# Optimization experiments

Measured on AMD Instinct MI355X. Metric: run time of the kernel, lower is better.

## Reference

```python
import jax, jax.numpy as jnp
import numpy as np

# Grid dimensions (match init_kwargs)
N_G = 100      # generators (grid['n_unit'])
N_LINE = 500   # transmission lines
N_LOAD = 200   # loads
N_BUS = 300    # buses
N_W = 50       # uncertainty sources (num_uncertainties)
N_SCEN = 128   # batch of realized-error scenarios (CvxpyLayer batch dim)
C_VIOL = 2.0e4 # violation penalty c_viol
N_ITERS = 600  # PDHG iterations for the batched LP solve
POWER_ITERS = 50


def _one_hot_nodes(key, n_items, n_bus):
    # incidence matrix [n_bus, n_items]: each item attached to one random bus
    idx = jax.random.randint(key, (n_items,), 0, n_bus)
    return jax.nn.one_hot(idx, n_bus, dtype=jnp.float32).T


def setup_inputs() -> dict:
    key = jax.random.key(0)
    ks = jax.random.split(key, 12)
    Pmax = 1.0 + 4.0 * jax.random.uniform(ks[0], (N_G,), dtype=jnp.float32)
    p_da = 0.8 * Pmax * jax.random.uniform(ks[1], (N_G,), dtype=jnp.float32)
    r_up_hat = jax.random.uniform(ks[2], (N_G,), dtype=jnp.float32)
    r_down_hat = jax.random.uniform(ks[3], (N_G,), dtype=jnp.float32)
    f_margin_up_hat = 5.0 + 5.0 * jax.random.uniform(ks[4], (N_LINE,), dtype=jnp.float32)
    f_margin_down_hat = 5.0 + 5.0 * jax.random.uniform(ks[5], (N_LINE,), dtype=jnp.float32)
    PTDF = 0.2 * jax.random.normal(ks[6], (N_LINE, N_BUS), dtype=jnp.float32)
    node_G = _one_hot_nodes(ks[7], N_G, N_BUS)
    node_L = _one_hot_nodes(ks[8], N_LOAD, N_BUS)
    node_W = _one_hot_nodes(ks[9], N_W, N_BUS)
    w_error_scen = 0.1 * jax.random.normal(ks[10], (N_SCEN, N_W), dtype=jnp.float32)
    return dict(p_da=p_da, r_up_hat=r_up_hat, r_down_hat=r_down_hat,
                f_margin_up_hat=f_margin_up_hat, f_margin_down_hat=f_margin_down_hat,
                w_error_scen=w_error_scen, Pmax=Pmax, PTDF=PTDF,
                node_G=node_G, node_L=node_L, node_W=node_W)


def _rt_clearing(p_da, r_up_hat, r_down_hat, f_up_hat, f_down_hat, w, Pmax, PTDF, node_G, node_L, node_W):
    # --- projection clamps (exactly as in torch forward) ---
    zero = jnp.zeros((), jnp.float32)
    r_up = jnp.maximum(jnp.minimum(r_up_hat, Pmax - p_da), zero)
    r_down = jnp.maximum(jnp.minimum(r_down_hat, p_da), zero)
    f_up = jnp.maximum(f_up_hat, zero)
    f_down = jnp.maximum(f_down_hat, zero)

    # --- reduced flow-sensitivity matrices ---
    Hg = PTDF @ node_G   # [L, G]
    Hl = PTDF @ node_L   # [L, D]
    Hw = PTDF @ node_W   # [L, W]

    G, D, L = N_G, N_LOAD, N_LINE
    n = 3 * G + D                 # x = [r_up_rec, r_down_rec, g_shed, l_shed]
    m = 2 * G + 2 * L + 1         # ineq rows + 1 equality (power balance)

    I = jnp.eye(G, dtype=jnp.float32)
    Zgg = jnp.zeros((G, G), jnp.float32)
    Zgd = jnp.zeros((G, D), jnp.float32)
    row1 = jnp.concatenate([I, Zgg, Zgg, Zgd], axis=1)          # ru <= r_up
    row2 = jnp.concatenate([Zgg, I, Zgg, Zgd], axis=1)          # rd <= r_down
    row3 = jnp.concatenate([Hg, -Hg, -Hg, Hl], axis=1)          # flow up
    row4 = -row3                                                # flow down
    og = jnp.ones((1, G), jnp.float32); od = jnp.ones((1, D), jnp.float32)
    row5 = jnp.concatenate([og, -og, -og, od], axis=1)          # balance (equality)
    K = jnp.concatenate([row1, row2, row3, row4, row5], axis=0)  # [m, n]

    c = C_VIOL * jnp.concatenate([jnp.zeros(2 * G, jnp.float32), jnp.ones(G + D, jnp.float32)])

    # per-scenario RHS q: Kx <= q (rows :-1), Kx == q (last row)
    S = w.shape[0]
    wH = w @ Hw.T  # [S, L]
    q = jnp.concatenate([
        jnp.broadcast_to(r_up, (S, G)),
        jnp.broadcast_to(r_down, (S, G)),
        f_up[None, :] - wH,
        f_down[None, :] + wH,
        -jnp.sum(w, axis=1, keepdims=True),
    ], axis=1)  # [S, m]

    # spectral norm of K via power iteration (step sizes)
    v = jnp.ones((n,), jnp.float32) / np.sqrt(n)
    s = jnp.ones((), jnp.float32)
    for _ in range(POWER_ITERS):
        v = K.T @ (K @ v)
        s = jnp.linalg.norm(v)
        v = v / s
    Lnorm = jnp.sqrt(s)
    step = 0.9 / Lnorm  # tau = sigma = step, tau*sigma*||K||^2 < 1

    ineq_mask = (jnp.arange(m) < m - 1)  # last row is equality: dual unprojected

    def pdhg_step(carry, _):
        x, y = carry
        x1 = jnp.maximum(x - step * (c + y @ K), 0.0)           # primal: x >= 0
        xb = 2.0 * x1 - x
        y1 = y + step * (xb @ K.T - q)
        y1 = jnp.where(ineq_mask, jnp.maximum(y1, 0.0), y1)     # dual: y_ineq >= 0
        return (x1, y1), None

    x0 = jnp.zeros((S, n), jnp.float32)
    y0 = jnp.zeros((S, m), jnp.float32)
    (xf, _), _ = jax.lax.scan(pdhg_step, (x0, y0), None, length=N_ITERS)

    g_shed = xf[:, 2 * G:3 * G]
    l_shed = xf[:, 3 * G:]
    cost_RT = C_VIOL * (jnp.sum(g_shed, axis=1) + jnp.sum(l_shed, axis=1))
    return cost_RT[:, None]  # [S, 1], matches cvxpy cost_RT variable


def reference(p_da, r_up_hat, r_down_hat, f_margin_up_hat, f_margin_down_hat,
              w_error_scen, Pmax, PTDF, node_G, node_L, node_W):
    return _rt_clearing(p_da, r_up_hat, r_down_hat, f_margin_up_hat, f_margin_down_hat,
                        w_error_scen, Pmax, PTDF, node_G, node_L, node_W)
```

## Files before the change

### kernel.cpp

```cpp
#include <hip/hip_runtime.h>
#include <hip/hip_fp16.h>
#include <math.h>

#define NG 100
#define ND 200
#define NLINE 500
#define NB 300
#define NW 50
#define NS 128
#define NX 500
#define CVIOL 20000.0f
#define NITERS 600
#define PITERS 50
#define NUPAD_MAX 304

#define NC   13
#define NUC  208

#define OFF_HSPB 0
#define OFF_HST  114688
#define OFF_B    270336
#define OFF_HWT  360336
#define OFF_QC   385336
#define OFF_QD   449336
#define OFF_RUP  513336
#define OFF_RDN  513436
#define OFF_FUP  513536
#define OFF_FDN  514036
#define OFF_QE   514536
#define OFF_STEP 514664
#define OFF_NU   514665
#define OFF_NUP  514666
#define OFF_NUC  514667
#define OFF_BUS  514668
#define OFF_BUSW 514968
#define OFF_UBUS 515018
#define OFF_C2U  515322
#define OFF_CUS  515622
#define OFF_CUL  515927

union f16pair { unsigned int u; _Float16 h[2]; };
__device__ __forceinline__ float h2lo(unsigned int x){ f16pair p; p.u = x; return (float)p.h[0]; }
__device__ __forceinline__ float h2hi(unsigned int x){ f16pair p; p.u = x; return (float)p.h[1]; }

__global__ __launch_bounds__(512) void k_pre(
    const float* __restrict__ p_da, const float* __restrict__ r_up_hat,
    const float* __restrict__ r_down_hat, const float* __restrict__ fup_hat,
    const float* __restrict__ fdn_hat, const float* __restrict__ w_err,
    const float* __restrict__ Pmax, const float* __restrict__ nG,
    const float* __restrict__ nL, const float* __restrict__ nW, float* ws) {
  __shared__ int busL[NB];
  __shared__ int uidxL[NB];
  __shared__ int cntL[NUPAD_MAX];
  __shared__ int ubusL[NUPAD_MAX];
  __shared__ int c2uL[NB];
  __shared__ int cusL[NUPAD_MAX + 1];
  __shared__ int culL[NB];
  const int t = threadIdx.x;
  int* busW = (int*)(ws + OFF_BUSW);
  if (t < NG) {
    int bf = 0;
    for (int b = 0; b < NB; ++b) if (nG[b*NG + t] > 0.5f) bf = b;
    busL[t] = bf;
    ws[OFF_RUP + t] = fmaxf(fminf(r_up_hat[t], Pmax[t] - p_da[t]), 0.f);
    ws[OFF_RDN + t] = fmaxf(fminf(r_down_hat[t], p_da[t]), 0.f);
  }
  if (t < ND) {
    int bf = 0;
    for (int b = 0; b < NB; ++b) if (nL[b*ND + t] > 0.5f) bf = b;
    busL[NG + t] = bf;
  }
  if (t < NW) {
    int bf = 0;
    for (int b = 0; b < NB; ++b) if (nW[b*NW + t] > 0.5f) bf = b;
    busW[t] = bf;
  }
  if (t < NLINE) {
    ws[OFF_FUP + t] = fmaxf(fup_hat[t], 0.f);
    ws[OFF_FDN + t] = fmaxf(fdn_hat[t], 0.f);
  }
  if (t < NS) {
    float s = 0.f;
    for (int w = 0; w < NW; ++w) s += w_err[t*NW + w];
    ws[OFF_QE + t] = -s;
  }
  __syncthreads();
  if (t == 0) {
    for (int b = 0; b < NB; ++b) uidxL[b] = -1;
    int nu = 0;
    for (int c = 0; c < NB; ++c) {
      const int b = busL[c];
      if (uidxL[b] < 0) { uidxL[b] = nu; ubusL[nu] = b; nu++; }
      c2uL[c] = uidxL[b];
    }
    for (int u = nu; u < NUPAD_MAX; ++u) ubusL[u] = 0;
    ((int*)(ws + OFF_NU))[0]  = nu;
    ((int*)(ws + OFF_NUP))[0] = (nu + 31) & ~31;
    ((int*)(ws + OFF_NUC))[0] = (nu <= NUC) ? NUC : 0;
    for (int u = 0; u < NUPAD_MAX; ++u) cntL[u] = 0;
    for (int c = 0; c < NB; ++c) cntL[c2uL[c]]++;
    int acc = 0;
    for (int u = 0; u < nu; ++u) { cusL[u] = acc; acc += cntL[u]; cntL[u] = cusL[u]; }
    for (int u = nu; u <= NUPAD_MAX; ++u) { if (u < NUPAD_MAX + 1) cusL[u] = acc; }
    for (int c = 0; c < NB; ++c) culL[cntL[c2uL[c]]++] = c;
  }
  __syncthreads();
  if (t < NUPAD_MAX) ((int*)(ws + OFF_UBUS))[t] = ubusL[t];
  if (t < NUPAD_MAX + 1) ((int*)(ws + OFF_CUS))[t] = cusL[t];
  if (t < NB) {
    ((int*)(ws + OFF_C2U))[t] = c2uL[t];
    ((int*)(ws + OFF_CUL))[t] = culL[t];
  }
}

__global__ __launch_bounds__(512) void k_buildH(const float* __restrict__ PTDF, float* ws) {
  const int l = blockIdx.x;
  const int t = threadIdx.x;
  const int NU   = ((const int*)(ws + OFF_NU))[0];
  const int NUCr = ((const int*)(ws + OFF_NUC))[0];
  const int* ubus = (const int*)(ws + OFF_UBUS);
  const int* busW = (const int*)(ws + OFF_BUSW);
  unsigned short* hb = (unsigned short*)(ws + OFF_HSPB);
  if (t < NUPAD_MAX) {
    const float val = (t < NU) ? PTDF[l*NB + ubus[t]] : 0.f;
    ws[OFF_HST + t*512 + l] = val;
    if (l == 0) {
      for (int ll = NLINE; ll < 512; ++ll) ws[OFF_HST + t*512 + ll] = 0.f;
    }
    if (NUCr > 0 && t < NUCr) {
      const int jp = l >> 6, half = (l >> 5) & 1, rg = l & 31;
      const unsigned short bv = __half_as_ushort(__float2half(val));
      hb[((((jp*NUC + t) << 5) + rg) << 1) + half] = bv;
      if (l == 0) {
        for (int rr = 20; rr < 32; ++rr)
          hb[((((7*NUC + t) << 5) + rr) << 1) + 1] = 0;
      }
    }
  } else if (t < NUPAD_MAX + NW) {
    const int w = t - NUPAD_MAX;
    ws[OFF_HWT + w*NLINE + l] = PTDF[l*NB + busW[w]];
  }
}

__global__ __launch_bounds__(192) void k_buildB(float* ws) {
  const int e = blockIdx.x;
  const int j = threadIdx.x;
  if (j >= 152) return;
  const float* __restrict__ re  = ws + OFF_HST + e*512;
  const float* __restrict__ rf0 = ws + OFF_HST + (2*j)*512;
  const float* __restrict__ rf1 = rf0 + 512;
  float a0 = 0.f, a1 = 0.f;
  #pragma unroll 4
  for (int l = 0; l < NLINE; ++l) {
    const float rv = re[l];
    a0 = fmaf(rv, rf0[l], a0);
    a1 = fmaf(rv, rf1[l], a1);
  }
  const unsigned int pk = (unsigned int)__half_as_ushort(__float2half(a0)) |
                          ((unsigned int)__half_as_ushort(__float2half(a1)) << 16);
  ((unsigned int*)(ws + OFF_B))[e*152 + j] = pk;
}

__global__ __launch_bounds__(512) void k_power(float* ws) {
  __shared__ unsigned int BuL[208*105];
  __shared__ __align__(16) float v[512];
  __shared__ float q3[NB];
  __shared__ __align__(16) float busq[NUPAD_MAX];
  __shared__ float gq[416];
  __shared__ int c2uL[NB], cusL[NUPAD_MAX + 1], culL[NB];
  __shared__ float sEs, sSs;
  const int t = threadIdx.x;
  const int NUCr = ((const int*)(ws + OFF_NUC))[0];
  const bool small = (NUCr == NUC);
  const unsigned int* __restrict__ BuPk = (const unsigned int*)(ws + OFF_B);
  if (small) {
    for (int i = t; i < 208*104; i += 512)
      BuL[(i/104)*105 + (i%104)] = BuPk[(i/104)*152 + (i%104)];
  }
  if (t < NB) { c2uL[t] = ((const int*)(ws + OFF_C2U))[t]; culL[t] = ((const int*)(ws + OFF_CUL))[t]; }
  if (t < NUPAD_MAX + 1) cusL[t] = ((const int*)(ws + OFF_CUS))[t];
  v[t] = (t < NX) ? (1.0f / sqrtf(500.0f)) : 0.f;
  __syncthreads();
  float s_last = 1.f;
  for (int it = 0; it < PITERS; ++it) {
    if (t < NG) q3[t] = v[t] - v[t + NG] - v[t + 2*NG];
    else if (t < NB) q3[t] = v[t + 200];
    __syncthreads();
    if (t < NUPAD_MAX) {
      float a = 0.f;
      const int ke = cusL[t + 1];
      for (int kk = cusL[t]; kk < ke; ++kk) {
        const int c = culL[kk];
        a += (c < NG) ? (q3[c] - q3[NG + c] - q3[2*NG + c]) : q3[200 + c];
      }
      busq[t] = a;
    }
    __syncthreads();
    if (small) {
      if (t < 416) {
        const int u = (t < 208) ? t : t - 208;
        const int p0 = (t < 208) ? 0 : 52;
        float a = 0.f;
        const unsigned int* row = BuL + u*105;
        #pragma unroll 4
        for (int p = p0; p < p0 + 52; ++p) {
          const unsigned int bu = row[p];
          const float2 bq = *(const float2*)&busq[2*p];
          a = fmaf(h2lo(bu), bq.x, fmaf(h2hi(bu), bq.y, a));
        }
        gq[t] = a;
      }
    } else {
      if (t < NUPAD_MAX) {
        float a = 0.f;
        const unsigned int* row = BuPk + t*152;
        for (int p = 0; p < 152; ++p) {
          const unsigned int bu = row[p];
          const float2 bq = *(const float2*)&busq[2*p];
          a = fmaf(h2lo(bu), bq.x, fmaf(h2hi(bu), bq.y, a));
        }
        gq[t] = a;
      }
    }
    if (t >= 448) {
      const int lane = t - 448;
      float e = 0.f;
      for (int idx = lane; idx < NB; idx += 64) e += q3[idx];
      for (int o = 32; o; o >>= 1) e += __shfl_down(e, o);
      if (lane == 0) sEs = e;
    }
    __syncthreads();
    if (t < NX) {
      const float E = sEs;
      const int ci = (t < NG) ? t : ((t < 2*NG) ? t - NG : ((t < NB) ? t - 2*NG : t - 200));
      const int ux = c2uL[ci];
      const float bq = small ? (gq[ux] + gq[208 + ux]) : gq[ux];
      float nv;
      if (t < NG)        nv = v[t] + 2.f*bq + E;
      else if (t < 2*NG) nv = v[t] - 2.f*bq - E;
      else if (t < NB)   nv = -2.f*bq - E;
      else               nv = 2.f*bq + E;
      v[t] = nv;
    }
    __syncthreads();
    if (t < 64) {
      float p = 0.f;
      for (int k = t; k < NX; k += 64) p += v[k]*v[k];
      for (int o = 32; o; o >>= 1) p += __shfl_down(p, o);
      if (t == 0) sSs = p;
    }
    __syncthreads();
    const float sn = sqrtf(sSs);
    if (t < NX) v[t] /= sn;
    s_last = sn;
    __syncthreads();
  }
  if (t == 0) ws[OFF_STEP] = 0.9f / sqrtf(s_last);
}

__global__ __launch_bounds__(512) void k_buildq(const float* __restrict__ w_err, float* ws) {
  const int s = blockIdx.x;
  const int t = threadIdx.x;
  __shared__ float wsh[NW];
  if (t < NW) wsh[t] = w_err[s*NW + t];
  __syncthreads();
  if (t < NLINE) {
    float wh = 0.f;
    #pragma unroll
    for (int w = 0; w < NW; ++w)
      wh = fmaf(wsh[w], ws[OFF_HWT + w*NLINE + t], wh);
    ws[OFF_QC + s*NLINE + t] = ws[OFF_FUP + t] - wh;
    ws[OFF_QD + s*NLINE + t] = ws[OFF_FDN + t] + wh;
  }
}

#define ROWKR(M,jp) M(jp,0) M(jp,1) M(jp,2) M(jp,3) M(jp,4) M(jp,5) M(jp,6) M(jp,7)
#define JPLIST(M) M(0) M(1) M(2) M(3) M(4) M(5) M(6) M(7)
#define KLIST(M)  M(0) M(1) M(2) M(3) M(4) M(5) M(6) M(7) M(8) M(9) M(10) M(11) M(12)

#define DECLH(jp,k) unsigned int h##jp##_##k;
#define DECLROW(jp) ROWKR(DECLH,jp)
#define LDH(jp,k)   h##jp##_##k = hpu[((((jp)*NUC) + cbase + (k)) << 5) + rg];
#define LDROW(jp)   ROWKR(LDH,jp)

#define ACCD(k)     float acc##k = 0.f;
#define DOTA(h, k)  acc##k = fmaf(h2lo(h), uu0, fmaf(h2hi(h), uu1, acc##k));
#define PHA(jp)     { const unsigned int upk = u_pk[rg + ((jp) << 5)]; \
                      const float uu0 = h2lo(upk), uu1 = h2hi(upk); \
                      DOTA(h##jp##_0, 0) DOTA(h##jp##_1, 1) DOTA(h##jp##_2, 2) DOTA(h##jp##_3, 3) \
                      DOTA(h##jp##_4, 4) DOTA(h##jp##_5, 5) DOTA(h##jp##_6, 6) DOTA(h##jp##_7, 7) \
                      const uint4 q4 = hx4[((jp) << 9) + t]; \
                      DOTA(q4.x, 8) DOTA(q4.y, 9) DOTA(q4.z, 10) DOTA(q4.w, 11) \
                      const unsigned int q1 = hx1[((jp) << 9) + t]; \
                      DOTA(q1, 12) }

#define TS16(k)     acc##k += __shfl_xor(acc##k, 16);
#define TRED(j)     tv##j += __shfl_xor(tv##j, 8); tv##j += __shfl_xor(tv##j, 4); \
                    tv##j += __shfl_xor(tv##j, 2); tv##j += __shfl_xor(tv##j, 1);

#define BRD(k)      const unsigned int _lo##k = __builtin_amdgcn_readlane(bzu, (k)); \
                    const unsigned int _hi##k = __builtin_amdgcn_readlane(bzu, 32 + (k)); \
                    const float b##k = __uint_as_float((t & 32) ? _hi##k : _lo##k);

#define CMC(h, k)   fx = fmaf(h2lo(h), b##k, fx); fy = fmaf(h2hi(h), b##k, fy);
#define PHC(jp)     { float fx = 0.f, fy = 0.f; \
                      CMC(h##jp##_0, 0) CMC(h##jp##_1, 1) CMC(h##jp##_2, 2) CMC(h##jp##_3, 3) \
                      CMC(h##jp##_4, 4) CMC(h##jp##_5, 5) CMC(h##jp##_6, 6) CMC(h##jp##_7, 7) \
                      const uint4 q4 = hx4[((jp) << 9) + t]; \
                      CMC(q4.x, 8) CMC(q4.y, 9) CMC(q4.z, 10) CMC(q4.w, 11) \
                      const unsigned int q1 = hx1[((jp) << 9) + t]; \
                      CMC(q1, 12) \
                      fx += __shfl_xor(fx, 32); fy += __shfl_xor(fy, 32); \
                      if ((t & 32) == 0) fpart2[w][rg + ((jp) << 5)] = make_float2(fx, fy); }

__global__ __launch_bounds__(512) void k_pdhg_reg(const float* __restrict__ ws,
                                                  float* __restrict__ out) {
  const int NUCr = ((const int*)(ws + OFF_NUC))[0];
  if (NUCr != NUC) return;

  __shared__ uint4 hx4[8*512];
  __shared__ unsigned int hx1[8*512];
  __shared__ unsigned int u_pk[256];
  __shared__ __align__(16) float x_s[512], z_s[512];
  __shared__ float ts[NUC];
  __shared__ __align__(16) float2 fpart2[8][256];
  __shared__ __align__(16) float2 qC2[256], qD2[256], yC2[256], yD2[256];
  __shared__ float yA[NG], yB[NG], qA[NG], qB[NG];
  __shared__ float sYE[1];
  __shared__ int c2u_s[NB], cus_s[NUPAD_MAX + 1], cul_s[NB];

  const int t = threadIdx.x;
  const int s = blockIdx.x;
  const int rg = t & 31, cg = t >> 5, w = t >> 6;
  const int cbase = cg * NC;
  const float step = ws[OFF_STEP];
  const float qE = ws[OFF_QE + s];

  x_s[t] = 0.f; z_s[t] = 0.f;
  if (t < 256) {
    const int l = (t & 31) + ((t >> 5) << 6);
    const float qc0 = (l < NLINE)      ? ws[OFF_QC + s*NLINE + l]      : 0.f;
    const float qc1 = (l + 32 < NLINE) ? ws[OFF_QC + s*NLINE + l + 32] : 0.f;
    const float qd0 = (l < NLINE)      ? ws[OFF_QD + s*NLINE + l]      : 0.f;
    const float qd1 = (l + 32 < NLINE) ? ws[OFF_QD + s*NLINE + l + 32] : 0.f;
    qC2[t] = make_float2(qc0, qc1); qD2[t] = make_float2(qd0, qd1);
    yC2[t] = make_float2(0.f, 0.f); yD2[t] = make_float2(0.f, 0.f);
    u_pk[t] = 0u;
  }
  if (t < NG) { yA[t] = 0.f; yB[t] = 0.f; qA[t] = ws[OFF_RUP + t]; qB[t] = ws[OFF_RDN + t]; }
  if (t < NB) {
    c2u_s[t] = ((const int*)(ws + OFF_C2U))[t];
    cul_s[t] = ((const int*)(ws + OFF_CUL))[t];
  }
  if (t < NUPAD_MAX + 1) cus_s[t] = ((const int*)(ws + OFF_CUS))[t];
  if (t == 0) sYE[0] = 0.f;

  JPLIST(DECLROW)
  {
    const unsigned int* __restrict__ hpu = (const unsigned int*)(ws + OFF_HSPB);
    JPLIST(LDROW)
    #pragma unroll
    for (int jp = 0; jp < 8; ++jp) {
      hx4[(jp << 9) + t] = make_uint4(
        hpu[((jp*NUC + cbase +  8) << 5) + rg],
        hpu[((jp*NUC + cbase +  9) << 5) + rg],
        hpu[((jp*NUC + cbase + 10) << 5) + rg],
        hpu[((jp*NUC + cbase + 11) << 5) + rg]);
      hx1[(jp << 9) + t] = hpu[((jp*NUC + cbase + 12) << 5) + rg];
    }
  }
  __syncthreads();

  for (int it = 0; it < NITERS; ++it) {
    {
      KLIST(ACCD)
      JPLIST(PHA)
      KLIST(TS16)
      const bool up16 = (t & 16) != 0;
      float tv0 = up16 ? acc7  : acc0;
      float tv1 = up16 ? acc8  : acc1;
      float tv2 = up16 ? acc9  : acc2;
      float tv3 = up16 ? acc10 : acc3;
      float tv4 = up16 ? acc11 : acc4;
      float tv5 = up16 ? acc12 : acc5;
      float tv6 = acc6;
      TRED(0) TRED(1) TRED(2) TRED(3) TRED(4) TRED(5) TRED(6)
      const int jsel = t & 15;
      float wv = tv0;
      wv = (jsel == 1) ? tv1 : wv; wv = (jsel == 2) ? tv2 : wv;
      wv = (jsel == 3) ? tv3 : wv; wv = (jsel == 4) ? tv4 : wv;
      wv = (jsel == 5) ? tv5 : wv; wv = (jsel == 6) ? tv6 : wv;
      const int kout = up16 ? (jsel + 7) : jsel;
      if (up16 ? (jsel < 6) : (jsel < 7)) ts[cbase + kout] = wv;
    }
    __syncthreads();

    if (t < NX) {
      const int cc = (t < NB) ? (t % NG) : (t - 200);
      const float tg = ts[c2u_s[cc]];
      const float yE = sYE[0];
      float yK;
      if (t < NG)        yK = yA[t] + tg + yE;
      else if (t < 2*NG) yK = yB[t - NG] - tg - yE;
      else if (t < NB)   yK = -tg - yE;
      else               yK = tg + yE;
      const float cj = (t < 2*NG) ? 0.f : CVIOL;
      const float xo = x_s[t];
      const float x1 = fmaxf(xo - step*(cj + yK), 0.f);
      z_s[t] = 2.f*x1 - xo;
      x_s[t] = x1;
    }
    __syncthreads();

    {
      float bz = 0.f;
      if (rg < NC) {
        const int c = cbase + rg;
        const int ke = cus_s[c + 1];
        float a = 0.f;
        for (int kk = cus_s[c]; kk < ke; ++kk) {
          const int comp = cul_s[kk];
          a += (comp < NG) ? (z_s[comp] - z_s[NG + comp] - z_s[2*NG + comp])
                           : z_s[200 + comp];
        }
        bz = a;
      }
      const unsigned int bzu = __float_as_uint(bz);
      KLIST(BRD)
      JPLIST(PHC)
    }
    __syncthreads();

    if (t < 256) {
      float2 cv = make_float2(0.f, 0.f);
      #pragma unroll
      for (int g = 0; g < 8; ++g) { const float2 fp = fpart2[g][t]; cv.x += fp.x; cv.y += fp.y; }
      const float2 qc = qC2[t], qd = qD2[t], yc = yC2[t], yd = yD2[t];
      const float cy0 = fmaxf(yc.x + step*( cv.x - qc.x), 0.f);
      const float dy0 = fmaxf(yd.x + step*(-cv.x - qd.x), 0.f);
      const float cy1 = fmaxf(yc.y + step*( cv.y - qc.y), 0.f);
      const float dy1 = fmaxf(yd.y + step*(-cv.y - qd.y), 0.f);
      yC2[t] = make_float2(cy0, cy1); yD2[t] = make_float2(dy0, dy1);
      const unsigned int upk =
          (unsigned int)__half_as_ushort(__float2half(cy0 - dy0)) |
          ((unsigned int)__half_as_ushort(__float2half(cy1 - dy1)) << 16);
      u_pk[t] = upk;
    }
    if (t >= 256 && t < 456) {
      const int g = t - 256;
      if (g < NG) yA[g] = fmaxf(yA[g] + step*(z_s[g] - qA[g]), 0.f);
      else { const int gb = g - NG; yB[gb] = fmaxf(yB[gb] + step*(z_s[g] - qB[gb]), 0.f); }
    }
    if (t >= 448) {
      const int lane = t - 448;
      float e = 0.f;
      #pragma unroll
      for (int m = 0; m < 8; ++m) {
        const int idx = lane + (m << 6);
        const float zv = z_s[idx];
        e += (idx < NG || idx >= NB) ? zv : -zv;
      }
      e += __shfl_xor(e, 32); e += __shfl_xor(e, 16); e += __shfl_xor(e, 8);
      e += __shfl_xor(e, 4);  e += __shfl_xor(e, 2);  e += __shfl_xor(e, 1);
      if (t == 511) sYE[0] += step*(e - qE);
    }
    __syncthreads();
  }

  if (t < 64) {
    float p = 0.f;
    for (int k = 200 + t; k < NX; k += 64) p += x_s[k];
    for (int o = 32; o; o >>= 1) p += __shfl_down(p, o);
    if (t == 0) out[s] = CVIOL * p;
  }
}

__global__ __launch_bounds__(1024) void k_pdhg_fb(const float* __restrict__ ws,
                                                  float* __restrict__ out) {
  const int NUCr = ((const int*)(ws + OFF_NUC))[0];
  if (NUCr != 0) return;
  const int NUPr = ((const int*)(ws + OFF_NUP))[0];

  __shared__ float u_s[512], x_s[512], z_s[512], cv_s[512];
  __shared__ float ts[NUPAD_MAX], busz[NUPAD_MAX];
  __shared__ float yC[NLINE], yD[NLINE], qC[NLINE], qD[NLINE];
  __shared__ float yA[NG], yB[NG], qA[NG], qB[NG];
  __shared__ float sE[1], sYE[1];
  __shared__ int c2u_s[NB], cus_s[NUPAD_MAX + 1], cul_s[NB];

  const int t = threadIdx.x;
  const int s = blockIdx.x;
  const float step = ws[OFF_STEP];
  const float qE = ws[OFF_QE + s];
  const float* __restrict__ HST = ws + OFF_HST;

  if (t < 512) { u_s[t] = 0.f; x_s[t] = 0.f; z_s[t] = 0.f; }
  if (t < NLINE) {
    yC[t] = 0.f; yD[t] = 0.f;
    qC[t] = ws[OFF_QC + s*NLINE + t];
    qD[t] = ws[OFF_QD + s*NLINE + t];
  }
  if (t < NG) { yA[t] = 0.f; yB[t] = 0.f; qA[t] = ws[OFF_RUP + t]; qB[t] = ws[OFF_RDN + t]; }
  if (t < NB) {
    c2u_s[t] = ((const int*)(ws + OFF_C2U))[t];
    cul_s[t] = ((const int*)(ws + OFF_CUL))[t];
  }
  if (t < NUPAD_MAX + 1) cus_s[t] = ((const int*)(ws + OFF_CUS))[t];
  if (t == 0) { sE[0] = 0.f; sYE[0] = 0.f; }
  __syncthreads();

  const int w = t >> 6, lane = t & 63;

  for (int it = 0; it < NITERS; ++it) {
    for (int c = w; c < NUPr; c += 16) {
      float a = 0.f;
      #pragma unroll
      for (int m = 0; m < 8; ++m) { const int l = lane + (m << 6); a = fmaf(HST[c*512 + l], u_s[l], a); }
      a += __shfl_xor(a, 32); a += __shfl_xor(a, 16); a += __shfl_xor(a, 8);
      a += __shfl_xor(a, 4);  a += __shfl_xor(a, 2);  a += __shfl_xor(a, 1);
      if (lane == 0) ts[c] = a;
    }
    __syncthreads();
    if (t < NX) {
      const int cc = (t < NB) ? (t % NG) : (t - 200);
      const float tg = ts[c2u_s[cc]];
      const float yE = sYE[0];
      float yK;
      if (t < NG)        yK = yA[t] + tg + yE;
      else if (t < 2*NG) yK = yB[t - NG] - tg - yE;
      else if (t < NB)   yK = -tg - yE;
      else               yK = tg + yE;
      const float cj = (t < 2*NG) ? 0.f : CVIOL;
      const float xo = x_s[t];
      const float x1 = fmaxf(xo - step*(cj + yK), 0.f);
      z_s[t] = 2.f*x1 - xo;
      x_s[t] = x1;
    }
    __syncthreads();
    if (t < NUPr) {
      float a = 0.f;
      const int k0 = cus_s[t], k1 = cus_s[t + 1];
      for (int k = k0; k < k1; ++k) {
        const int c = cul_s[k];
        a += (c < NG) ? (z_s[c] - z_s[NG + c] - z_s[2*NG + c]) : z_s[200 + c];
      }
      busz[t] = a;
    } else if (t >= 768 && t < 832) {
      const int ln = t - 768;
      float e = 0.f;
      for (int idx = ln; idx < NX; idx += 64) {
        const float zv = z_s[idx];
        e += (idx < NG || idx >= NB) ? zv : -zv;
      }
      e += __shfl_xor(e, 32); e += __shfl_xor(e, 16); e += __shfl_xor(e, 8);
      e += __shfl_xor(e, 4);  e += __shfl_xor(e, 2);  e += __shfl_xor(e, 1);
      if (ln == 0) sE[0] = e;
    }
    __syncthreads();
    if (t < 512) {
      float a = 0.f;
      for (int c = 0; c < NUPr; ++c) a = fmaf(HST[c*512 + t], busz[c], a);
      cv_s[t] = a;
    }
    __syncthreads();
    if (t < NLINE) {
      const float cv = cv_s[t];
      const float cy = fmaxf(yC[t] + step*( cv - qC[t]), 0.f);
      const float dy = fmaxf(yD[t] + step*(-cv - qD[t]), 0.f);
      yC[t] = cy; yD[t] = dy; u_s[t] = cy - dy;
    } else if (t >= 512 && t < 612) {
      const int g = t - 512;
      yA[g] = fmaxf(yA[g] + step*(z_s[g] - qA[g]), 0.f);
    } else if (t >= 612 && t < 712) {
      const int g = t - 612;
      yB[g] = fmaxf(yB[g] + step*(z_s[NG + g] - qB[g]), 0.f);
    } else if (t == 1023) {
      sYE[0] += step*(sE[0] - qE);
    }
    __syncthreads();
  }
  if (t < 64) {
    float p = 0.f;
    for (int k = 200 + t; k < NX; k += 64) p += x_s[k];
    for (int o = 32; o; o >>= 1) p += __shfl_down(p, o);
    if (t == 0) out[s] = CVIOL * p;
  }
}

extern "C" void kernel_launch(void* const* d_in, const int* in_sizes, int n_in,
                              void* d_out, int out_size, void* d_ws, size_t ws_size,
                              hipStream_t stream) {
  (void)in_sizes; (void)n_in; (void)out_size; (void)ws_size;
  const float* p_da      = (const float*)d_in[0];
  const float* r_up_hat  = (const float*)d_in[1];
  const float* r_dn_hat  = (const float*)d_in[2];
  const float* fup_hat   = (const float*)d_in[3];
  const float* fdn_hat   = (const float*)d_in[4];
  const float* w_err     = (const float*)d_in[5];
  const float* Pmax      = (const float*)d_in[6];
  const float* PTDF      = (const float*)d_in[7];
  const float* nG        = (const float*)d_in[8];
  const float* nL        = (const float*)d_in[9];
  const float* nW        = (const float*)d_in[10];
  float* ws  = (float*)d_ws;
  float* out = (float*)d_out;

  hipLaunchKernelGGL(k_pre,    dim3(1),   dim3(512),  0, stream,
                     p_da, r_up_hat, r_dn_hat, fup_hat, fdn_hat, w_err, Pmax, nG, nL, nW, ws);
  hipLaunchKernelGGL(k_buildH, dim3(500), dim3(512),  0, stream, PTDF, ws);
  hipLaunchKernelGGL(k_buildB, dim3(304), dim3(192),  0, stream, ws);
  hipLaunchKernelGGL(k_power,  dim3(1),   dim3(512),  0, stream, ws);
  hipLaunchKernelGGL(k_buildq, dim3(128), dim3(512),  0, stream, w_err, ws);
  hipLaunchKernelGGL(k_pdhg_reg, dim3(128), dim3(512), 0, stream, ws, out);
  hipLaunchKernelGGL(k_pdhg_fb, dim3(128), dim3(1024), 0, stream, ws, out);
}
```

Before: 2.780 ms.

## Use packed fp16 dot2 in PDHG matvec and keep column 12 in registers

The A-phase dot products now use the packed fp16 dot2 intrinsic (v_dot2_f32_f16) when it is available. This replaces two conversions plus two FMAs per packed element with a single instruction. The 13th column of each row pair moves from LDS into registers, which removes the hx1 shared array and one LDS load per row pair in both phases. The change adds 8 registers per thread, raising pressure at 512 threads. dot2 also takes u in fp16 rather than converting it to fp32 first, which may change rounding.

```diff
diff --git a/kernel.cpp b/kernel.cpp
--- a/kernel.cpp
+++ b/kernel.cpp
@@ -39,9 +39,17 @@
 #define OFF_CUS  515622
 #define OFF_CUL  515927
 
-union f16pair { unsigned int u; _Float16 h[2]; };
+typedef _Float16 half2v __attribute__((ext_vector_type(2)));
+union f16pair { unsigned int u; _Float16 h[2]; half2v v; };
 __device__ __forceinline__ float h2lo(unsigned int x){ f16pair p; p.u = x; return (float)p.h[0]; }
 __device__ __forceinline__ float h2hi(unsigned int x){ f16pair p; p.u = x; return (float)p.h[1]; }
+__device__ __forceinline__ half2v h2v(unsigned int x){ f16pair p; p.u = x; return p.v; }
+
+#if defined(__has_builtin)
+#if __has_builtin(__builtin_amdgcn_fdot2)
+#define HAVE_FDOT2 1
+#endif
+#endif
 
 __global__ __launch_bounds__(512) void k_pre(
     const float* __restrict__ p_da, const float* __restrict__ r_up_hat,
@@ -278,21 +286,29 @@
 #define JPLIST(M) M(0) M(1) M(2) M(3) M(4) M(5) M(6) M(7)
 #define KLIST(M)  M(0) M(1) M(2) M(3) M(4) M(5) M(6) M(7) M(8) M(9) M(10) M(11) M(12)
 
-#define DECLH(jp,k) unsigned int h##jp##_##k;
-#define DECLROW(jp) ROWKR(DECLH,jp)
-#define LDH(jp,k)   h##jp##_##k = hpu[((((jp)*NUC) + cbase + (k)) << 5) + rg];
-#define LDROW(jp)   ROWKR(LDH,jp)
+#define DECLH(jp,k) unsigned int hr##jp##_##k;
+#define DECLROW(jp) ROWKR(DECLH,jp) DECLH(jp,12)
+#define LDH(jp,k)   hr##jp##_##k = hpu[((((jp)*NUC) + cbase + (k)) << 5) + rg];
+#define LDROW(jp)   ROWKR(LDH,jp) LDH(jp,12)
 
 #define ACCD(k)     float acc##k = 0.f;
-#define DOTA(h, k)  acc##k = fmaf(h2lo(h), uu0, fmaf(h2hi(h), uu1, acc##k));
-#define PHA(jp)     { const unsigned int upk = u_pk[rg + ((jp) << 5)]; \
-                      const float uu0 = h2lo(upk), uu1 = h2hi(upk); \
-                      DOTA(h##jp##_0, 0) DOTA(h##jp##_1, 1) DOTA(h##jp##_2, 2) DOTA(h##jp##_3, 3) \
-                      DOTA(h##jp##_4, 4) DOTA(h##jp##_5, 5) DOTA(h##jp##_6, 6) DOTA(h##jp##_7, 7) \
-                      const uint4 q4 = hx4[((jp) << 9) + t]; \
-                      DOTA(q4.x, 8) DOTA(q4.y, 9) DOTA(q4.z, 10) DOTA(q4.w, 11) \
-                      const unsigned int q1 = hx1[((jp) << 9) + t]; \
-                      DOTA(q1, 12) }
+
+#ifdef HAVE_FDOT2
+#define DOTA(hv, k) acc##k = __builtin_amdgcn_fdot2(h2v(hv), uh2, acc##k, false);
+#else
+#define DOTA(hv, k) { const unsigned int hcu_ = (hv); \
+                      acc##k = fmaf(h2lo(hcu_), uu0, fmaf(h2hi(hcu_), uu1, acc##k)); }
+#endif
+
+#define PHA(jp)     { const unsigned int upk_ = u_pk[rg + ((jp) << 5)]; \
+                      const half2v uh2 = h2v(upk_); (void)uh2; \
+                      const float uu0 = h2lo(upk_), uu1 = h2hi(upk_); \
+                      (void)uu0; (void)uu1; \
+                      DOTA(hr##jp##_0, 0) DOTA(hr##jp##_1, 1) DOTA(hr##jp##_2, 2) DOTA(hr##jp##_3, 3) \
+                      DOTA(hr##jp##_4, 4) DOTA(hr##jp##_5, 5) DOTA(hr##jp##_6, 6) DOTA(hr##jp##_7, 7) \
+                      const uint4 q4_ = hx4[((jp) << 9) + t]; \
+                      DOTA(q4_.x, 8) DOTA(q4_.y, 9) DOTA(q4_.z, 10) DOTA(q4_.w, 11) \
+                      DOTA(hr##jp##_12, 12) }
 
 #define TS16(k)     acc##k += __shfl_xor(acc##k, 16);
 #define TRED(j)     tv##j += __shfl_xor(tv##j, 8); tv##j += __shfl_xor(tv##j, 4); \
@@ -302,14 +318,14 @@
                     const unsigned int _hi##k = __builtin_amdgcn_readlane(bzu, 32 + (k)); \
                     const float b##k = __uint_as_float((t & 32) ? _hi##k : _lo##k);
 
-#define CMC(h, k)   fx = fmaf(h2lo(h), b##k, fx); fy = fmaf(h2hi(h), b##k, fy);
+#define CMC(hv, k)  { const unsigned int hcu_ = (hv); \
+                      fx = fmaf(h2lo(hcu_), b##k, fx); fy = fmaf(h2hi(hcu_), b##k, fy); }
 #define PHC(jp)     { float fx = 0.f, fy = 0.f; \
-                      CMC(h##jp##_0, 0) CMC(h##jp##_1, 1) CMC(h##jp##_2, 2) CMC(h##jp##_3, 3) \
-                      CMC(h##jp##_4, 4) CMC(h##jp##_5, 5) CMC(h##jp##_6, 6) CMC(h##jp##_7, 7) \
-                      const uint4 q4 = hx4[((jp) << 9) + t]; \
-                      CMC(q4.x, 8) CMC(q4.y, 9) CMC(q4.z, 10) CMC(q4.w, 11) \
-                      const unsigned int q1 = hx1[((jp) << 9) + t]; \
-                      CMC(q1, 12) \
+                      CMC(hr##jp##_0, 0) CMC(hr##jp##_1, 1) CMC(hr##jp##_2, 2) CMC(hr##jp##_3, 3) \
+                      CMC(hr##jp##_4, 4) CMC(hr##jp##_5, 5) CMC(hr##jp##_6, 6) CMC(hr##jp##_7, 7) \
+                      const uint4 q4_ = hx4[((jp) << 9) + t]; \
+                      CMC(q4_.x, 8) CMC(q4_.y, 9) CMC(q4_.z, 10) CMC(q4_.w, 11) \
+                      CMC(hr##jp##_12, 12) \
                       fx += __shfl_xor(fx, 32); fy += __shfl_xor(fy, 32); \
                       if ((t & 32) == 0) fpart2[w][rg + ((jp) << 5)] = make_float2(fx, fy); }
 
@@ -319,7 +335,6 @@
   if (NUCr != NUC) return;
 
   __shared__ uint4 hx4[8*512];
-  __shared__ unsigned int hx1[8*512];
   __shared__ unsigned int u_pk[256];
   __shared__ __align__(16) float x_s[512], z_s[512];
   __shared__ float ts[NUC];
@@ -366,7 +381,6 @@
         hpu[((jp*NUC + cbase +  9) << 5) + rg],
         hpu[((jp*NUC + cbase + 10) << 5) + rg],
         hpu[((jp*NUC + cbase + 11) << 5) + rg]);
-      hx1[(jp << 9) + t] = hpu[((jp*NUC + cbase + 12) << 5) + rg];
     }
   }
   __syncthreads();
```

Measured after the change: 3.262 ms. 1.17x slower.
